# Kernel tuning notes

Hardware: AMD Instinct MI355X
Metric: run time of the kernel (lower is better)

Reference implementation:

```python
import jax, jax.numpy as jnp
import numpy as np

B, M, FIN, K, FOUT, NNZ = 8, 40000, 64, 6, 64, 320000

def setup_inputs() -> dict:
    key = jax.random.key(0)
    k1, k2, k3, k4, k5 = jax.random.split(key, 5)
    x = jax.random.normal(k1, (B, M, FIN), dtype=jnp.float32)
    edge_rows = jax.random.randint(k2, (NNZ,), 0, M)
    edge_cols = jax.random.randint(k3, (NNZ,), 0, M)
    edge_vals = jax.random.normal(k4, (NNZ,), dtype=jnp.float32) * 0.1
    W = jax.random.normal(k5, (FIN * K, FOUT), dtype=jnp.float32) * 0.05
    return {"x": x, "edge_vals": edge_vals, "W": W,
            "edge_rows": edge_rows, "edge_cols": edge_cols}

def reference(x, edge_vals, W, edge_rows, edge_cols):
    Bd, Md, Fin = x.shape
    nK = W.shape[0] // Fin
    Fout = W.shape[1]
    # x0: [M, Fin*B] as in tf.transpose([1,2,0]) + reshape
    x0 = jnp.transpose(x, (1, 2, 0)).reshape(Md, Fin * Bd)

    def spmm_rescaled(v):
        # rescale_L(L, lmax=2) = L - I, so (L - I) @ v = L@v - v
        Lv = jax.ops.segment_sum(edge_vals[:, None] * v[edge_cols],
                                 edge_rows, num_segments=Md)
        return Lv - v

    xs = [x0]
    if nK > 1:
        x1 = spmm_rescaled(x0)
        xs.append(x1)
        xp, xc = x0, x1
        for _ in range(2, nK):
            xn = 2.0 * spmm_rescaled(xc) - xp  # Chebyshev recurrence
            xs.append(xn)
            xp, xc = xc, xn
    X = jnp.stack(xs, axis=0)                     # [K, M, Fin*B]
    X = X.reshape(nK, Md, Fin, Bd)                # split Fin*B -> (Fin, B)
    X = jnp.transpose(X, (3, 1, 2, 0))            # [B, M, Fin, K]
    X = X.reshape(Bd * Md, Fin * nK)
    out = (X @ W).reshape(Bd, Md, Fout)           # dense projection
    return out
```

## Files before the change

### kernel.cpp

```cpp
#include <hip/hip_runtime.h>

#define Mn    40000
#define Bn    8
#define FINn  64
#define Kn    6
#define FOUTn 64
#define NNZn  320000
#define Cn    512
#define NB    ((Mn + 255) / 256)


typedef _Float16 half8 __attribute__((ext_vector_type(8)));
typedef __attribute__((ext_vector_type(4))) float floatx4;

__device__ __forceinline__ ushort f2h(float f) {
    _Float16 h = (_Float16)f;
    return *(ushort*)&h;
}


__global__ __launch_bounds__(256) void k_hist(const int* __restrict__ rows,
                                              int* __restrict__ cnt) {
    int e = blockIdx.x * 256 + threadIdx.x;
    if (e < NNZn) atomicAdd(&cnt[rows[e]], 1);
}

__global__ __launch_bounds__(256) void k_scan_part(const int* __restrict__ cnt,
                                                   int* __restrict__ rowptr,
                                                   int* __restrict__ bsum) {
    __shared__ int part[256];
    int tid = threadIdx.x;
    int r = blockIdx.x * 256 + tid;
    int v = (r < Mn) ? cnt[r] : 0;
    part[tid] = v;
    __syncthreads();
    for (int off = 1; off < 256; off <<= 1) {
        int t = (tid >= off) ? part[tid - off] : 0;
        __syncthreads();
        part[tid] += t;
        __syncthreads();
    }
    if (r < Mn) rowptr[r] = part[tid] - v;
    if (tid == 255) bsum[blockIdx.x] = part[255];
}

__global__ __launch_bounds__(256) void k_scan_bsums(const int* __restrict__ bsum,
                                                    int* __restrict__ boff,
                                                    int* __restrict__ rowptr) {
    __shared__ int part[256];
    int tid = threadIdx.x;
    int v = (tid < NB) ? bsum[tid] : 0;
    part[tid] = v;
    __syncthreads();
    for (int off = 1; off < 256; off <<= 1) {
        int t = (tid >= off) ? part[tid - off] : 0;
        __syncthreads();
        part[tid] += t;
        __syncthreads();
    }
    if (tid < NB) boff[tid] = part[tid] - v;
    if (tid == 255) rowptr[Mn] = part[255];
}

__global__ __launch_bounds__(256) void k_scan_add(int* __restrict__ rowptr,
                                                  const int* __restrict__ boff,
                                                  int* __restrict__ wcur) {
    int r = blockIdx.x * 256 + threadIdx.x;
    if (r < Mn) {
        int v = rowptr[r] + boff[blockIdx.x];
        rowptr[r] = v;
        wcur[r] = v;
    }
}

__global__ __launch_bounds__(256) void k_scatter(const int* __restrict__ rows,
                                                 const int* __restrict__ cols,
                                                 const float* __restrict__ vals,
                                                 int* __restrict__ wcur,
                                                 int2* __restrict__ csr) {
    int e = blockIdx.x * 256 + threadIdx.x;
    if (e < NNZn) {
        int p = atomicAdd(&wcur[rows[e]], 1);
        int2 cv; cv.x = cols[e]; cv.y = __float_as_int(vals[e]);
        csr[p] = cv;
    }
}


__global__ __launch_bounds__(256) void k_transpose_h(const float* __restrict__ x,
                                                     ushort* __restrict__ x0h) {
    size_t i = ((size_t)blockIdx.x * 256 + threadIdx.x) * 8;
    float4 a = *(const float4*)(x + i);
    float4 b = *(const float4*)(x + i + 4);
    union { uint4 u; ushort h[8]; } s;
    s.h[0] = f2h(a.x); s.h[1] = f2h(a.y); s.h[2] = f2h(a.z); s.h[3] = f2h(a.w);
    s.h[4] = f2h(b.x); s.h[5] = f2h(b.y); s.h[6] = f2h(b.z); s.h[7] = f2h(b.w);
    *(uint4*)(x0h + i) = s.u;
}


__device__ __forceinline__ void fmah8(float* a, uint4 g, float w) {
    union { uint4 u; _Float16 h[8]; } c; c.u = g;
#pragma unroll
    for (int i = 0; i < 8; ++i) a[i] += w * (float)c.h[i];
}

__global__ __launch_bounds__(256) void k_spmm_h(const ushort* __restrict__ xc,
                                                const ushort* __restrict__ xp,
                                                ushort* __restrict__ xn,
                                                const int* __restrict__ rowptr,
                                                const int2* __restrict__ csr,
                                                int first) {
    int t = threadIdx.x;
    int lane = t & 63;
    int m = blockIdx.x * 4 + (t >> 6);
    const uint4* xc4 = (const uint4*)xc;
    size_t loff = (size_t)(lane >> 3) * ((size_t)Mn * 8) + (lane & 7);
    uint4 v = xc4[loff + (size_t)m * 8];
    uint4 p;
    if (!first) p = ((const uint4*)xp)[loff + (size_t)m * 8];
    float a[8];
    { union { uint4 u; _Float16 h[8]; } c; c.u = v;
#pragma unroll
      for (int i = 0; i < 8; ++i) a[i] = -(float)c.h[i]; }

    int e = rowptr[m], end = rowptr[m + 1];
    for (; e + 8 <= end; e += 8) {
        int2 cv[8];
#pragma unroll
        for (int i = 0; i < 8; ++i) cv[i] = csr[e + i];
        uint4 g[8];
#pragma unroll
        for (int i = 0; i < 8; ++i) g[i] = xc4[loff + (size_t)cv[i].x * 8];
#pragma unroll
        for (int i = 0; i < 8; ++i) fmah8(a, g[i], __int_as_float(cv[i].y));
    }
    for (; e + 4 <= end; e += 4) {
        int2 cv0 = csr[e],     cv1 = csr[e + 1];
        int2 cv2 = csr[e + 2], cv3 = csr[e + 3];
        uint4 g0 = xc4[loff + (size_t)cv0.x * 8];
        uint4 g1 = xc4[loff + (size_t)cv1.x * 8];
        uint4 g2 = xc4[loff + (size_t)cv2.x * 8];
        uint4 g3 = xc4[loff + (size_t)cv3.x * 8];
        fmah8(a, g0, __int_as_float(cv0.y));
        fmah8(a, g1, __int_as_float(cv1.y));
        fmah8(a, g2, __int_as_float(cv2.y));
        fmah8(a, g3, __int_as_float(cv3.y));
    }
    for (; e < end; ++e) {
        int2 cv = csr[e];
        uint4 g = xc4[loff + (size_t)cv.x * 8];
        fmah8(a, g, __int_as_float(cv.y));
    }

    if (!first) {
        union { uint4 u; _Float16 h[8]; } c; c.u = p;
#pragma unroll
        for (int i = 0; i < 8; ++i) a[i] = 2.f * a[i] - (float)c.h[i];
    }
    union { uint4 u; _Float16 h[8]; } s;
#pragma unroll
    for (int i = 0; i < 8; ++i) s.h[i] = (_Float16)a[i];
    ((uint4*)xn)[loff + (size_t)m * 8] = s.u;
}


__global__ __launch_bounds__(256) void k_wfrag(const float* __restrict__ W,
                                               ushort* __restrict__ wfrag) {
    int idx = blockIdx.x * 256 + threadIdx.x;
    if (idx >= 12 * 4 * 64 * 8) return;
    int j    = idx & 7;
    int lane = (idx >> 3) & 63;
    int n    = (idx >> 9) & 3;
    int kk   = idx >> 11;
    int k    = (lane >> 4) * 8 + j;
    int lev  = kk >> 1;
    int f    = (kk & 1) * 32 + k;
    int fo   = n * 16 + (lane & 15);
    wfrag[idx] = f2h(W[(f * Kn + lev) * FOUTn + fo]);
}


__global__ __launch_bounds__(256, 2) void k_gemm_mfma(const ushort* __restrict__ xh,
                                                      const ushort* __restrict__ wfrag,
                                                      float* __restrict__ out) {
    int t    = threadIdx.x;
    int wv   = t >> 6;
    int lane = t & 63;
    int q    = lane >> 4, r = lane & 15;
    int b    = blockIdx.x & 7;
    int m0   = (blockIdx.x >> 3) * 64;

    const size_t lstrideH = (size_t)Bn * Mn * 64;
    const ushort* abase = xh + ((size_t)b * Mn + m0 + wv * 16 + r) * 64 + q * 8;

    half8 aA0 = *(const half8*)(abase);
    half8 aB0 = *(const half8*)(abase + 32);
    half8 aA1 = *(const half8*)(abase + 1 * lstrideH);
    half8 aB1 = *(const half8*)(abase + 1 * lstrideH + 32);
    half8 aA2 = *(const half8*)(abase + 2 * lstrideH);
    half8 aB2 = *(const half8*)(abase + 2 * lstrideH + 32);
    half8 aA3 = *(const half8*)(abase + 3 * lstrideH);
    half8 aB3 = *(const half8*)(abase + 3 * lstrideH + 32);
    half8 aA4 = *(const half8*)(abase + 4 * lstrideH);
    half8 aB4 = *(const half8*)(abase + 4 * lstrideH + 32);
    half8 aA5 = *(const half8*)(abase + 5 * lstrideH);
    half8 aB5 = *(const half8*)(abase + 5 * lstrideH + 32);

    floatx4 acc[4];
    acc[0] = (floatx4)0.f; acc[1] = (floatx4)0.f;
    acc[2] = (floatx4)0.f; acc[3] = (floatx4)0.f;

#define MC_HALF(kkg, af)                                                              \
    do {                                                                              \
        const ushort* wf = wfrag + ((size_t)((kkg) * 4) * 64 + lane) * 8;             \
        acc[0] = __builtin_amdgcn_mfma_f32_16x16x32_f16(af, *(const half8*)(wf),        acc[0], 0, 0, 0); \
        acc[1] = __builtin_amdgcn_mfma_f32_16x16x32_f16(af, *(const half8*)(wf + 512),  acc[1], 0, 0, 0); \
        acc[2] = __builtin_amdgcn_mfma_f32_16x16x32_f16(af, *(const half8*)(wf + 1024), acc[2], 0, 0, 0); \
        acc[3] = __builtin_amdgcn_mfma_f32_16x16x32_f16(af, *(const half8*)(wf + 1536), acc[3], 0, 0, 0); \
    } while (0)

    MC_HALF(0,  aA0); MC_HALF(1,  aB0);
    MC_HALF(2,  aA1); MC_HALF(3,  aB1);
    MC_HALF(4,  aA2); MC_HALF(5,  aB2);
    MC_HALF(6,  aA3); MC_HALF(7,  aB3);
    MC_HALF(8,  aA4); MC_HALF(9,  aB4);
    MC_HALF(10, aA5); MC_HALF(11, aB5);
#undef MC_HALF

    size_t obase = ((size_t)b * Mn + m0 + wv * 16) * FOUTn;
#pragma unroll
    for (int n = 0; n < 4; ++n) {
#pragma unroll
        for (int reg = 0; reg < 4; ++reg) {
            int orow = q * 4 + reg;
            out[obase + (size_t)orow * FOUTn + n * 16 + r] = acc[n][reg];
        }
    }
}


__global__ __launch_bounds__(512) void k_transpose_f(const float* __restrict__ x,
                                                     float* __restrict__ x0) {
    int m = blockIdx.x, t = threadIdx.x;
    int b = t >> 6, f = t & 63;
    x0[(size_t)m * Cn + t] = x[((size_t)b * Mn + m) * 64 + f];
}

__global__ __launch_bounds__(256) void k_spmm_f32(const float4* __restrict__ xc,
                                                  const float4* __restrict__ xp,
                                                  float4* __restrict__ xn,
                                                  const int* __restrict__ rowptr,
                                                  const int2* __restrict__ csr,
                                                  int first) {
    int t = threadIdx.x;
    int lane = t & 63;
    int m = blockIdx.x * 4 + (t >> 6);
    size_t rb = (size_t)m * 128;
    float4 v0 = xc[rb + lane];
    float4 v1 = xc[rb + 64 + lane];
    float4 a0 = make_float4(-v0.x, -v0.y, -v0.z, -v0.w);
    float4 a1 = make_float4(-v1.x, -v1.y, -v1.z, -v1.w);
    int e = rowptr[m], end = rowptr[m + 1];
    for (; e < end; ++e) {
        int2 cv = csr[e];
        float w = __int_as_float(cv.y);
        const float4* r = xc + (size_t)cv.x * 128;
        float4 g0 = r[lane], g1 = r[64 + lane];
        a0.x += w * g0.x; a0.y += w * g0.y; a0.z += w * g0.z; a0.w += w * g0.w;
        a1.x += w * g1.x; a1.y += w * g1.y; a1.z += w * g1.z; a1.w += w * g1.w;
    }
    if (!first) {
        float4 p0 = xp[rb + lane];
        float4 p1 = xp[rb + 64 + lane];
        a0.x = 2.f * a0.x - p0.x; a0.y = 2.f * a0.y - p0.y;
        a0.z = 2.f * a0.z - p0.z; a0.w = 2.f * a0.w - p0.w;
        a1.x = 2.f * a1.x - p1.x; a1.y = 2.f * a1.y - p1.y;
        a1.z = 2.f * a1.z - p1.z; a1.w = 2.f * a1.w - p1.w;
    }
    xn[rb + lane] = a0;
    xn[rb + 64 + lane] = a1;
}

__global__ __launch_bounds__(256) void k_gemm2(const float* __restrict__ xa,
                                               const float* __restrict__ xb,
                                               const float* __restrict__ W,
                                               float* __restrict__ out,
                                               int ka, int kb, int accum) {
    __shared__ __align__(16) float Wa[64 * 64];
    __shared__ __align__(16) float Wb[64 * 64];
    __shared__ __align__(16) float xsa[4 * Cn];
    __shared__ __align__(16) float xsb[4 * Cn];
    int t = threadIdx.x;
    size_t m0 = (size_t)blockIdx.x * 4;
    for (int i = t; i < 4096; i += 256) {
        int f = i >> 6, fo = i & 63;
        Wa[i] = W[(f * Kn + ka) * FOUTn + fo];
        Wb[i] = W[(f * Kn + kb) * FOUTn + fo];
    }
    for (int i = t; i < 4 * Cn; i += 256) {
        xsa[i] = xa[m0 * Cn + i];
        xsb[i] = xb[m0 * Cn + i];
    }
    __syncthreads();
    int fo  = (t & 15) * 4;
    int idx = t >> 4;
    int m   = idx & 3;
    int bq  = idx >> 2;
    float4 acc0 = make_float4(0.f, 0.f, 0.f, 0.f);
    float4 acc1 = make_float4(0.f, 0.f, 0.f, 0.f);
    for (int f = 0; f < 64; ++f) {
        float4 wa = *(const float4*)&Wa[f * 64 + fo];
        float a0 = xsa[m * Cn + bq * 64 + f];
        float a1 = xsa[m * Cn + (bq + 4) * 64 + f];
        acc0.x += a0 * wa.x; acc0.y += a0 * wa.y; acc0.z += a0 * wa.z; acc0.w += a0 * wa.w;
        acc1.x += a1 * wa.x; acc1.y += a1 * wa.y; acc1.z += a1 * wa.z; acc1.w += a1 * wa.w;
        float4 wb = *(const float4*)&Wb[f * 64 + fo];
        float b0 = xsb[m * Cn + bq * 64 + f];
        float b1 = xsb[m * Cn + (bq + 4) * 64 + f];
        acc0.x += b0 * wb.x; acc0.y += b0 * wb.y; acc0.z += b0 * wb.z; acc0.w += b0 * wb.w;
        acc1.x += b1 * wb.x; acc1.y += b1 * wb.y; acc1.z += b1 * wb.z; acc1.w += b1 * wb.w;
    }
    size_t o0 = (((size_t)bq * Mn) + (m0 + m)) * FOUTn + fo;
    size_t o1 = (((size_t)(bq + 4) * Mn) + (m0 + m)) * FOUTn + fo;
    float4* out4_0 = (float4*)&out[o0];
    float4* out4_1 = (float4*)&out[o1];
    if (accum) {
        float4 c0 = *out4_0, c1 = *out4_1;
        acc0.x += c0.x; acc0.y += c0.y; acc0.z += c0.z; acc0.w += c0.w;
        acc1.x += c1.x; acc1.y += c1.y; acc1.z += c1.z; acc1.w += c1.w;
    }
    *out4_0 = acc0;
    *out4_1 = acc1;
}


extern "C" void kernel_launch(void* const* d_in, const int* in_sizes, int n_in,
                              void* d_out, int out_size, void* d_ws, size_t ws_size,
                              hipStream_t stream) {
    const float* x         = (const float*)d_in[0];
    const float* edge_vals = (const float*)d_in[1];
    const float* W         = (const float*)d_in[2];
    const int*   edge_rows = (const int*)d_in[3];
    const int*   edge_cols = (const int*)d_in[4];
    float* out = (float*)d_out;

    char* ws = (char*)d_ws;
    const size_t bufB = (size_t)Mn * Cn * sizeof(float);
    const size_t bufH = (size_t)Mn * Cn * sizeof(ushort);
    const size_t wfB  = 12 * 4 * 64 * 8 * sizeof(ushort);
    const size_t csrB = (size_t)(Mn + 4 + Mn) * 4 + (size_t)NNZn * 8;

    const int spmm_grid = Mn / 4;
    const int gemm_grid = (Mn / 64) * 8;

    if (ws_size >= 6 * bufH + wfB + csrB) {
        ushort* xh  = (ushort*)ws;
        ushort* wfr = (ushort*)(ws + 6 * bufH);
        int*    rowptr = (int*)(ws + 6 * bufH + wfB);
        int*    fill   = rowptr + (Mn + 4);
        int2*   csr    = (int2*)(fill + Mn);
        int*    bsum   = (int*)csr;
        int*    boff   = bsum + 256;
        ushort* slot[6];
        for (int l = 0; l < 6; ++l) slot[l] = xh + (size_t)l * Mn * Cn;

        hipMemsetAsync(fill, 0, Mn * sizeof(int), stream);
        k_hist<<<(NNZn + 255) / 256, 256, 0, stream>>>(edge_rows, fill);
        k_scan_part<<<NB, 256, 0, stream>>>(fill, rowptr, bsum);
        k_scan_bsums<<<1, 256, 0, stream>>>(bsum, boff, rowptr);
        k_scan_add<<<NB, 256, 0, stream>>>(rowptr, boff, fill);
        k_scatter<<<(NNZn + 255) / 256, 256, 0, stream>>>(edge_rows, edge_cols,
                                                          edge_vals, fill, csr);
        k_wfrag<<<96, 256, 0, stream>>>(W, wfr);

        k_transpose_h<<<(Bn * Mn * FINn) / (256 * 8), 256, 0, stream>>>(x, slot[0]);
        k_spmm_h<<<spmm_grid, 256, 0, stream>>>(slot[0], slot[0], slot[1],
                                                rowptr, csr, 1);
        k_spmm_h<<<spmm_grid, 256, 0, stream>>>(slot[1], slot[0], slot[2],
                                                rowptr, csr, 0);
        k_spmm_h<<<spmm_grid, 256, 0, stream>>>(slot[2], slot[1], slot[3],
                                                rowptr, csr, 0);
        k_spmm_h<<<spmm_grid, 256, 0, stream>>>(slot[3], slot[2], slot[4],
                                                rowptr, csr, 0);
        k_spmm_h<<<spmm_grid, 256, 0, stream>>>(slot[4], slot[3], slot[5],
                                                rowptr, csr, 0);
        k_gemm_mfma<<<gemm_grid, 256, 0, stream>>>(xh, wfr, out);
    } else {
        float* buf0 = (float*)(ws);
        float* buf1 = (float*)(ws + bufB);
        float* buf2 = (float*)(ws + 2 * bufB);
        int*   rowptr = (int*)(ws + 3 * bufB);
        int*   fill   = rowptr + (Mn + 4);
        int2*  csr    = (int2*)(fill + Mn);
        int*   bsum   = (int*)csr;
        int*   boff   = bsum + 256;
        hipMemsetAsync(fill, 0, Mn * sizeof(int), stream);
        k_hist<<<(NNZn + 255) / 256, 256, 0, stream>>>(edge_rows, fill);
        k_scan_part<<<NB, 256, 0, stream>>>(fill, rowptr, bsum);
        k_scan_bsums<<<1, 256, 0, stream>>>(bsum, boff, rowptr);
        k_scan_add<<<NB, 256, 0, stream>>>(rowptr, boff, fill);
        k_scatter<<<(NNZn + 255) / 256, 256, 0, stream>>>(edge_rows, edge_cols,
                                                          edge_vals, fill, csr);
        k_transpose_f<<<Mn, 512, 0, stream>>>(x, buf0);
        k_spmm_f32<<<spmm_grid, 256, 0, stream>>>((const float4*)buf0, (const float4*)buf0,
                                                  (float4*)buf1, rowptr, csr, 1);
        k_gemm2<<<Mn / 4, 256, 0, stream>>>(buf0, buf1, W, out, 0, 1, 0);
        k_spmm_f32<<<spmm_grid, 256, 0, stream>>>((const float4*)buf1, (const float4*)buf0,
                                                  (float4*)buf2, rowptr, csr, 0);
        k_spmm_f32<<<spmm_grid, 256, 0, stream>>>((const float4*)buf2, (const float4*)buf1,
                                                  (float4*)buf0, rowptr, csr, 0);
        k_gemm2<<<Mn / 4, 256, 0, stream>>>(buf2, buf0, W, out, 2, 3, 1);
        k_spmm_f32<<<spmm_grid, 256, 0, stream>>>((const float4*)buf0, (const float4*)buf2,
                                                  (float4*)buf1, rowptr, csr, 0);
        k_spmm_f32<<<spmm_grid, 256, 0, stream>>>((const float4*)buf1, (const float4*)buf0,
                                                  (float4*)buf2, rowptr, csr, 0);
        k_gemm2<<<Mn / 4, 256, 0, stream>>>(buf1, buf2, W, out, 4, 5, 1);
    }
}
```

Baseline: 571.0 us.

## Store Chebyshev levels row-major so each SpMM gather reads one contiguous row

Changes the fp16 intermediate layout from batch-major [B][M][64] to node-major [M][B*64]. Each gathered neighbour row in the SpMM then becomes a single contiguous 1 KB read per wavefront instead of eight separate 128 B segments spread across batch planes. The transpose kernel now writes the interleaved layout and the MFMA GEMM indexes it, with a new block-to-(batch, tile) mapping and a sched_barrier after the A loads. The cost is strided writes in the transpose and a different GEMM access pattern.

Measured after the change: 543.8 us. 1.05x faster.

```diff
diff --git a/kernel.cpp b/kernel.cpp
--- a/kernel.cpp
+++ b/kernel.cpp
@@ -8,6 +8,7 @@
 #define NNZn  320000
 #define Cn    512
 #define NB    ((Mn + 255) / 256)
+#define MT    (Mn / 64)
 
 
 typedef _Float16 half8 __attribute__((ext_vector_type(8)));
@@ -89,13 +90,20 @@
 
 __global__ __launch_bounds__(256) void k_transpose_h(const float* __restrict__ x,
                                                      ushort* __restrict__ x0h) {
-    size_t i = ((size_t)blockIdx.x * 256 + threadIdx.x) * 8;
-    float4 a = *(const float4*)(x + i);
-    float4 b = *(const float4*)(x + i + 4);
-    union { uint4 u; ushort h[8]; } s;
-    s.h[0] = f2h(a.x); s.h[1] = f2h(a.y); s.h[2] = f2h(a.z); s.h[3] = f2h(a.w);
-    s.h[4] = f2h(b.x); s.h[5] = f2h(b.y); s.h[6] = f2h(b.z); s.h[7] = f2h(b.w);
-    *(uint4*)(x0h + i) = s.u;
+    int m0 = blockIdx.x * 4;
+    int t  = threadIdx.x;
+#pragma unroll
+    for (int k = 0; k < 2; ++k) {
+        int i   = t + k * 256;
+        int ml  = i >> 7;
+        int rem = i & 127;
+        int b   = rem >> 4;
+        int fq  = (rem & 15) * 4;
+        float4 a = *(const float4*)(x + ((size_t)b * Mn + m0 + ml) * 64 + fq);
+        union { uint2 u; ushort h[4]; } s;
+        s.h[0] = f2h(a.x); s.h[1] = f2h(a.y); s.h[2] = f2h(a.z); s.h[3] = f2h(a.w);
+        *(uint2*)(x0h + (size_t)(m0 + ml) * Cn + b * 64 + fq) = s.u;
+    }
 }
 
 
@@ -115,10 +123,9 @@
     int lane = t & 63;
     int m = blockIdx.x * 4 + (t >> 6);
     const uint4* xc4 = (const uint4*)xc;
-    size_t loff = (size_t)(lane >> 3) * ((size_t)Mn * 8) + (lane & 7);
-    uint4 v = xc4[loff + (size_t)m * 8];
+    uint4 v = xc4[(size_t)m * 64 + lane];
     uint4 p;
-    if (!first) p = ((const uint4*)xp)[loff + (size_t)m * 8];
+    if (!first) p = ((const uint4*)xp)[(size_t)m * 64 + lane];
     float a[8];
     { union { uint4 u; _Float16 h[8]; } c; c.u = v;
 #pragma unroll
@@ -131,17 +138,17 @@
         for (int i = 0; i < 8; ++i) cv[i] = csr[e + i];
         uint4 g[8];
 #pragma unroll
-        for (int i = 0; i < 8; ++i) g[i] = xc4[loff + (size_t)cv[i].x * 8];
+        for (int i = 0; i < 8; ++i) g[i] = xc4[(size_t)cv[i].x * 64 + lane];
 #pragma unroll
         for (int i = 0; i < 8; ++i) fmah8(a, g[i], __int_as_float(cv[i].y));
     }
     for (; e + 4 <= end; e += 4) {
         int2 cv0 = csr[e],     cv1 = csr[e + 1];
         int2 cv2 = csr[e + 2], cv3 = csr[e + 3];
-        uint4 g0 = xc4[loff + (size_t)cv0.x * 8];
-        uint4 g1 = xc4[loff + (size_t)cv1.x * 8];
-        uint4 g2 = xc4[loff + (size_t)cv2.x * 8];
-        uint4 g3 = xc4[loff + (size_t)cv3.x * 8];
+        uint4 g0 = xc4[(size_t)cv0.x * 64 + lane];
+        uint4 g1 = xc4[(size_t)cv1.x * 64 + lane];
+        uint4 g2 = xc4[(size_t)cv2.x * 64 + lane];
+        uint4 g3 = xc4[(size_t)cv3.x * 64 + lane];
         fmah8(a, g0, __int_as_float(cv0.y));
         fmah8(a, g1, __int_as_float(cv1.y));
         fmah8(a, g2, __int_as_float(cv2.y));
@@ -149,7 +156,7 @@
     }
     for (; e < end; ++e) {
         int2 cv = csr[e];
-        uint4 g = xc4[loff + (size_t)cv.x * 8];
+        uint4 g = xc4[(size_t)cv.x * 64 + lane];
         fmah8(a, g, __int_as_float(cv.y));
     }
 
@@ -161,7 +168,7 @@
     union { uint4 u; _Float16 h[8]; } s;
 #pragma unroll
     for (int i = 0; i < 8; ++i) s.h[i] = (_Float16)a[i];
-    ((uint4*)xn)[loff + (size_t)m * 8] = s.u;
+    ((uint4*)xn)[(size_t)m * 64 + lane] = s.u;
 }
 
 
@@ -184,15 +191,16 @@
 __global__ __launch_bounds__(256, 2) void k_gemm_mfma(const ushort* __restrict__ xh,
                                                       const ushort* __restrict__ wfrag,
                                                       float* __restrict__ out) {
-    int t    = threadIdx.x;
-    int wv   = t >> 6;
-    int lane = t & 63;
-    int q    = lane >> 4, r = lane & 15;
-    int b    = blockIdx.x & 7;
-    int m0   = (blockIdx.x >> 3) * 64;
-
-    const size_t lstrideH = (size_t)Bn * Mn * 64;
-    const ushort* abase = xh + ((size_t)b * Mn + m0 + wv * 16 + r) * 64 + q * 8;
+    int t     = threadIdx.x;
+    int wv    = t >> 6;
+    int lane  = t & 63;
+    int q     = lane >> 4, r = lane & 15;
+    int mtile = blockIdx.x % MT;
+    int b     = blockIdx.x / MT;
+    int m0    = mtile * 64;
+
+    const size_t lstrideH = (size_t)Mn * Cn;
+    const ushort* abase = xh + (size_t)(m0 + wv * 16 + r) * Cn + b * 64 + q * 8;
 
     half8 aA0 = *(const half8*)(abase);
     half8 aB0 = *(const half8*)(abase + 32);
@@ -206,6 +214,7 @@
     half8 aB4 = *(const half8*)(abase + 4 * lstrideH + 32);
     half8 aA5 = *(const half8*)(abase + 5 * lstrideH);
     half8 aB5 = *(const half8*)(abase + 5 * lstrideH + 32);
+    __builtin_amdgcn_sched_barrier(0);
 
     floatx4 acc[4];
     acc[0] = (floatx4)0.f; acc[1] = (floatx4)0.f;
@@ -352,7 +361,7 @@
     const size_t csrB = (size_t)(Mn + 4 + Mn) * 4 + (size_t)NNZn * 8;
 
     const int spmm_grid = Mn / 4;
-    const int gemm_grid = (Mn / 64) * 8;
+    const int gemm_grid = MT * 8;
 
     if (ws_size >= 6 * bufH + wfB + csrB) {
         ushort* xh  = (ushort*)ws;
@@ -374,7 +383,7 @@
                                                           edge_vals, fill, csr);
         k_wfrag<<<96, 256, 0, stream>>>(W, wfr);
 
-        k_transpose_h<<<(Bn * Mn * FINn) / (256 * 8), 256, 0, stream>>>(x, slot[0]);
+        k_transpose_h<<<Mn / 4, 256, 0, stream>>>(x, slot[0]);
         k_spmm_h<<<spmm_grid, 256, 0, stream>>>(slot[0], slot[0], slot[1],
                                                 rowptr, csr, 1);
         k_spmm_h<<<spmm_grid, 256, 0, stream>>>(slot[1], slot[0], slot[2],
```
